# Optimization experiments

Measured on AMD Instinct MI355X. Metric: run time of the kernel, lower is better.

The kernel has to match this reference:

```python
import jax, jax.numpy as jnp
import numpy as np

RADIUS = 3.4
NSAMPLE = 5


def setup_inputs() -> dict:
    key = jax.random.key(0)
    x = jax.random.normal(key, (8, 4096, 3), dtype=jnp.float32)
    return {"x": x}


def reference(x) -> jnp.ndarray:
    # pointnet2 ball_query(radius=3.4, nsample=5, xyz=x, new_xyz=x)
    # For each query point, take the first NSAMPLE point indices (in scan order)
    # with squared distance < radius^2; if fewer than NSAMPLE found, remaining
    # slots hold the FIRST found index (CUDA kernel fills row with first hit).
    r2 = jnp.float32(RADIUS * RADIUS)
    sq = jnp.sum(x * x, axis=-1)  # [B, N]
    # d2[b, q, k] = ||x_q - x_k||^2
    d2 = sq[:, :, None] + sq[:, None, :] - 2.0 * jnp.einsum("bqd,bkd->bqk", x, x)
    mask = d2 < r2  # [B, Nq, N]
    # 0-based rank of each True entry along the scan axis
    cum = jnp.cumsum(mask.astype(jnp.int32), axis=-1)
    rank = cum - mask.astype(jnp.int32)  # rank among hits, valid where mask
    first_idx = jnp.argmax(mask, axis=-1).astype(jnp.int32)  # [B, Nq] (0 if none)
    slots = []
    for j in range(NSAMPLE):
        sel = mask & (rank == j)
        has_j = jnp.any(sel, axis=-1)
        idx_j = jnp.argmax(sel, axis=-1).astype(jnp.int32)
        slots.append(jnp.where(has_j, idx_j, first_idx))
    return jnp.stack(slots, axis=-1)  # [B, Nq, NSAMPLE] int32
```

## Files before the change

kernel.cpp:

```cpp
#include <hip/hip_runtime.h>


#pragma clang fp contract(off)

#define BQ_N 4096
#define BQ_B 8
#define BQ_NS 5

__global__ __launch_bounds__(1024) void ball_query_kernel(
    const float* __restrict__ x, int* __restrict__ out, float r2) {
  const int wid = (blockIdx.x * 1024 + threadIdx.x) >> 6;
  const int lane = threadIdx.x & 63;
  const int b = wid >> 12;
  const int q = wid & (BQ_N - 1);

  const float* xb = x + (size_t)b * BQ_N * 3;

  const float qx = xb[q * 3 + 0];
  const float qy = xb[q * 3 + 1];
  const float qz = xb[q * 3 + 2];
  const float kx0 = xb[lane * 3 + 0];
  const float ky0 = xb[lane * 3 + 1];
  const float kz0 = xb[lane * 3 + 2];

  const float sq_q = (qx * qx + qy * qy) + qz * qz;
  const float sqk0 = (kx0 * kx0 + ky0 * ky0) + kz0 * kz0;
  const float dot0 = (qx * kx0 + qy * ky0) + qz * kz0;
  const float d20 = (sq_q + sqk0) - 2.0f * dot0;

  const int base = wid * BQ_NS;
  const unsigned long long below = ((unsigned long long)1 << lane) - 1ull;

  const unsigned long long m1 = __ballot(d20 < r2);
  if (d20 < r2) {
    const int rank = __popcll(m1 & below);
    if (rank < BQ_NS) out[base + rank] = lane;
  }
  int cnt = __popcll(m1);

  if (cnt < BQ_NS) {
    int first = (m1 != 0ull) ? (__ffsll((long long)m1) - 1) : -1;
    for (int k0 = 64; k0 < BQ_N && cnt < BQ_NS; k0 += 64) {
      const int k = k0 + lane;
      const float kx = xb[k * 3 + 0];
      const float ky = xb[k * 3 + 1];
      const float kz = xb[k * 3 + 2];
      const float sqk = (kx * kx + ky * ky) + kz * kz;
      const float dot = (qx * kx + qy * ky) + qz * kz;
      const float d2 = (sq_q + sqk) - 2.0f * dot;
      const bool h = d2 < r2;
      const unsigned long long m = __ballot(h);
      if (h) {
        const int rank = cnt + __popcll(m & below);
        if (rank < BQ_NS) out[base + rank] = k;
      }
      if (first < 0 && m != 0ull) first = k0 + __ffsll((long long)m) - 1;
      cnt += __popcll(m);
    }
    if (lane == 0 && cnt < BQ_NS) {
      for (int j = (cnt < 1 ? 1 : cnt); j < BQ_NS; ++j) out[base + j] = first;
    }
  }
}

extern "C" void kernel_launch(void* const* d_in, const int* in_sizes, int n_in,
                              void* d_out, int out_size, void* d_ws, size_t ws_size,
                              hipStream_t stream) {
  const float* x = (const float*)d_in[0];
  int* out = (int*)d_out;
  const float r2 = 3.4f * 3.4f;

  const int total_waves = BQ_B * BQ_N;
  const int block = 1024;
  const int grid = total_waves / 16;
  ball_query_kernel<<<grid, block, 0, stream>>>(x, out, r2);
}
```

Measured before the change: 56.16 us.

## Pack four queries per wavefront using 16-lane subgroups

Each 64-lane wavefront now serves four query points, with each 16-lane group scanning candidates 16 at a time, in place of one query per wave scanning 64 at a time. With radius 3.4 on normal data nearly every point is a hit, so most queries finish in the first chunk and the old scheme left most lanes idle. This cuts the wave count by four. The cost is that a wave keeps looping until all four queries have their samples, and each chunk now covers fewer candidates.

```diff
diff --git a/kernel.cpp b/kernel.cpp
--- a/kernel.cpp
+++ b/kernel.cpp
@@ -11,53 +11,59 @@
     const float* __restrict__ x, int* __restrict__ out, float r2) {
   const int wid = (blockIdx.x * 1024 + threadIdx.x) >> 6;
   const int lane = threadIdx.x & 63;
-  const int b = wid >> 12;
-  const int q = wid & (BQ_N - 1);
+  const int group = lane >> 4;
+  const int sub = lane & 15;
+
+  const int qidx = wid * 4 + group;
+  const int b = qidx >> 12;
+  const int q = qidx & (BQ_N - 1);
 
   const float* xb = x + (size_t)b * BQ_N * 3;
 
   const float qx = xb[q * 3 + 0];
   const float qy = xb[q * 3 + 1];
   const float qz = xb[q * 3 + 2];
-  const float kx0 = xb[lane * 3 + 0];
-  const float ky0 = xb[lane * 3 + 1];
-  const float kz0 = xb[lane * 3 + 2];
+  const float kx0 = xb[sub * 3 + 0];
+  const float ky0 = xb[sub * 3 + 1];
+  const float kz0 = xb[sub * 3 + 2];
 
   const float sq_q = (qx * qx + qy * qy) + qz * qz;
   const float sqk0 = (kx0 * kx0 + ky0 * ky0) + kz0 * kz0;
   const float dot0 = (qx * kx0 + qy * ky0) + qz * kz0;
   const float d20 = (sq_q + sqk0) - 2.0f * dot0;
 
-  const int base = wid * BQ_NS;
-  const unsigned long long below = ((unsigned long long)1 << lane) - 1ull;
+  const int base = qidx * BQ_NS;
+  const unsigned sublow = (1u << sub) - 1u;
 
   const unsigned long long m1 = __ballot(d20 < r2);
+  const unsigned mg1 = (unsigned)(m1 >> (group * 16)) & 0xFFFFu;
   if (d20 < r2) {
-    const int rank = __popcll(m1 & below);
-    if (rank < BQ_NS) out[base + rank] = lane;
+    const int rank = __popc(mg1 & sublow);
+    if (rank < BQ_NS) out[base + rank] = sub;
   }
-  int cnt = __popcll(m1);
+  int cnt = __popc(mg1);
 
-  if (cnt < BQ_NS) {
-    int first = (m1 != 0ull) ? (__ffsll((long long)m1) - 1) : -1;
-    for (int k0 = 64; k0 < BQ_N && cnt < BQ_NS; k0 += 64) {
-      const int k = k0 + lane;
+  if (__any(cnt < BQ_NS)) {
+    int first = (mg1 != 0u) ? (__ffs(mg1) - 1) : -1;
+    for (int k0 = 16; k0 < BQ_N && __any(cnt < BQ_NS); k0 += 16) {
+      const int k = k0 + sub;
       const float kx = xb[k * 3 + 0];
       const float ky = xb[k * 3 + 1];
       const float kz = xb[k * 3 + 2];
       const float sqk = (kx * kx + ky * ky) + kz * kz;
       const float dot = (qx * kx + qy * ky) + qz * kz;
       const float d2 = (sq_q + sqk) - 2.0f * dot;
-      const bool h = d2 < r2;
-      const unsigned long long m = __ballot(h);
-      if (h) {
-        const int rank = cnt + __popcll(m & below);
+      const bool h = (d2 < r2) && (cnt < BQ_NS + 16);
+      const unsigned long long m = __ballot(d2 < r2);
+      const unsigned mg = (unsigned)(m >> (group * 16)) & 0xFFFFu;
+      if (h && cnt < BQ_NS) {
+        const int rank = cnt + __popc(mg & sublow);
         if (rank < BQ_NS) out[base + rank] = k;
       }
-      if (first < 0 && m != 0ull) first = k0 + __ffsll((long long)m) - 1;
-      cnt += __popcll(m);
+      if (first < 0 && mg != 0u) first = k0 + __ffs(mg) - 1;
+      if (cnt < BQ_NS) cnt += __popc(mg);
     }
-    if (lane == 0 && cnt < BQ_NS) {
+    if (sub == 0 && cnt < BQ_NS) {
       for (int j = (cnt < 1 ? 1 : cnt); j < BQ_NS; ++j) out[base + j] = first;
     }
   }
@@ -70,7 +76,7 @@
   int* out = (int*)d_out;
   const float r2 = 3.4f * 3.4f;
 
-  const int total_waves = BQ_B * BQ_N;
+  const int total_waves = (BQ_B * BQ_N) / 4;
   const int block = 1024;
   const int grid = total_waves / 16;
   ball_query_kernel<<<grid, block, 0, stream>>>(x, out, r2);
```

Result: no change. 55.11 us (-1.9%).
